# Kernel tuning notes

Measured on AMD Instinct MI355X. Metric: run time of the kernel, lower is better.

Reference implementation:

```python
import jax, jax.numpy as jnp
import numpy as np

B, D = 4, 4            # batch, days
N = 5000               # node_number
V = 256                # congestion_space_dimension
F = 64                 # in_channels
C = 32                 # out_channels per head
H = 4                  # heads
E = 80000              # edges per graph (before self loops)
NEG_SLOPE = 0.2        # PyG GATConv default negative_slope


def setup_inputs() -> dict:
    key = jax.random.key(0)
    ks = jax.random.split(key, 7)
    x = jax.random.randint(ks[0], (B, D, N), 0, V)
    adjacency = jax.random.randint(ks[1], (2, E), 0, N)
    emb = jax.random.normal(ks[2], (V, F), dtype=jnp.float32)
    W = jax.random.normal(ks[3], (F, H * C), dtype=jnp.float32) * 0.1
    att_src = jax.random.normal(ks[4], (H, C), dtype=jnp.float32) * 0.1
    att_dst = jax.random.normal(ks[5], (H, C), dtype=jnp.float32) * 0.1
    bias = jnp.zeros((H * C,), dtype=jnp.float32)
    return {"x": x, "adjacency": adjacency, "emb": emb, "W": W,
            "att_src": att_src, "att_dst": att_dst, "bias": bias}


def reference(x, adjacency, emb, W, att_src, att_dst, bias):
    G = B * D
    feats = emb[x].reshape(G, N, F)                       # [G,N,F] embedding lookup
    # PyG GATConv adds self loops by default
    loops = jnp.arange(N)
    src = jnp.concatenate([adjacency[0], loops])          # [Et]
    dst = jnp.concatenate([adjacency[1], loops])          # [Et]
    xw = jnp.einsum('gnf,fk->gnk', feats, W).reshape(G, N, H, C)
    a_s = jnp.einsum('gnhc,hc->gnh', xw, att_src)         # [G,N,H]
    a_d = jnp.einsum('gnhc,hc->gnh', xw, att_dst)
    e = jax.nn.leaky_relu(a_s[:, src] + a_d[:, dst], NEG_SLOPE)  # [G,Et,H]
    # per-destination segment softmax (stable)
    seg_max = jax.vmap(lambda v: jax.ops.segment_max(v, dst, num_segments=N))(e)
    alpha = jnp.exp(e - seg_max[:, dst])
    denom = jax.vmap(lambda v: jax.ops.segment_sum(v, dst, num_segments=N))(alpha)
    alpha = alpha / denom[:, dst]                         # [G,Et,H]
    msg = alpha[..., None] * xw[:, src]                   # [G,Et,H,C]
    out = jax.vmap(lambda m: jax.ops.segment_sum(m, dst, num_segments=N))(msg)
    out = out.reshape(G, N, H * C) + bias                 # concat heads + bias
    return out.reshape(B, D, N * H * C)
```

## Files before the change

kernel.cpp:

```cpp
#include <hip/hip_runtime.h>
#include <math.h>

#define NN 5000
#define GG 16
#define VV 256
#define FF 64
#define HH 4
#define CC 32
#define HC 128
#define EE 80000
#define NEG 0.2f
#define WPB 4
#define SLOT 48
#define SPAD 50
#define CAP 96
#define NTASK (GG * NN / 4)

__global__ void k_tables(const float* __restrict__ emb, const float* __restrict__ W,
                         const float* __restrict__ att_src, const float* __restrict__ att_dst,
                         float* __restrict__ T, float* __restrict__ as_t, float* __restrict__ ad_t,
                         int* __restrict__ cursor, int* __restrict__ csr) {
  if (blockIdx.x >= VV) {
    int n = (blockIdx.x - VV) * 128 + threadIdx.x;
    if (n < NN) {
      cursor[n] = 1;
      csr[n * CAP] = n;
    }
    return;
  }
  __shared__ float se[FF];
  __shared__ float sT[HC];
  const int v = blockIdx.x;
  const int k = threadIdx.x;
  if (k < FF) se[k] = emb[v * FF + k];
  __syncthreads();
  float acc = 0.f;
#pragma unroll
  for (int f = 0; f < FF; ++f) acc += se[f] * W[f * HC + k];
  T[v * HC + k] = acc;
  sT[k] = acc;
  __syncthreads();
  if (k < 2 * HH) {
    const int h = k >> 1;
    const float* att = (k & 1) ? att_dst : att_src;
    float s = 0.f;
#pragma unroll
    for (int c = 0; c < CC; ++c) s += sT[h * CC + c] * att[h * CC + c];
    if (k & 1) ad_t[v * HH + h] = s;
    else       as_t[v * HH + h] = s;
  }
}

#define NSCAT ((EE + 255) / 256)
__global__ void k_scatter_p(const int* __restrict__ src, const int* __restrict__ dst,
                            int* __restrict__ cursor, int* __restrict__ csr,
                            const float* __restrict__ as_t, const float* __restrict__ ad_t,
                            float* __restrict__ P) {
  if (blockIdx.x < NSCAT) {
    int e = blockIdx.x * 256 + threadIdx.x;
    if (e < EE) {
      int d = dst[e];
      int pos = atomicAdd(&cursor[d], 1);
      if (pos < CAP) csr[d * CAP + pos] = src[e];
    }
    return;
  }
  const int d = blockIdx.x - NSCAT;
  const int v = threadIdx.x;
  const float4 a = ((const float4*)as_t)[v];
  const float4 b = ((const float4*)ad_t)[d];
  float e0 = a.x + b.x; e0 = e0 > 0.f ? e0 : NEG * e0;
  float e1 = a.y + b.y; e1 = e1 > 0.f ? e1 : NEG * e1;
  float e2 = a.z + b.z; e2 = e2 > 0.f ? e2 : NEG * e2;
  float e3 = a.w + b.w; e3 = e3 > 0.f ? e3 : NEG * e3;
  float4 p;
  p.x = __expf(e0); p.y = __expf(e1); p.z = __expf(e2); p.w = __expf(e3);
  ((float4*)P)[d * VV + v] = p;
}

__global__ __launch_bounds__(256)
void k_gat(const int* __restrict__ x, const int* __restrict__ cursor,
           const int* __restrict__ csr, const float* __restrict__ T,
           const float* __restrict__ P, const float* __restrict__ bias,
           float* __restrict__ out) {
  __shared__ float4 s_p4[WPB][4][SPAD];
  __shared__ int    s_ofs[WPB][4][SPAD];

  const int tid  = threadIdx.x;
  const int wave = tid >> 6;
  const int lane = tid & 63;
  const int sub  = lane >> 4;
  const int sl   = lane & 15;
  const int head = sl >> 2;

  const int w    = blockIdx.x * WPB + wave;
  const int inst = w * 4 + sub;
  const int g    = inst / NN;
  const int n    = inst - g * NN;

  const int base = n * CAP;
  const int deg  = min(cursor[n], CAP);
  const int xd   = x[inst];
  const float4* __restrict__ Pd = ((const float4*)P) + xd * VV;
  const int* __restrict__ xg = x + g * NN;

  const int my_ch = sl * 8;
  const float4 b0 = ((const float4*)bias)[sl * 2];
  const float4 b1 = ((const float4*)bias)[sl * 2 + 1];

  float4 dsum = make_float4(0.f, 0.f, 0.f, 0.f);
  float4 a0 = make_float4(0.f, 0.f, 0.f, 0.f);
  float4 a1 = make_float4(0.f, 0.f, 0.f, 0.f);

  for (int c0 = 0; c0 < deg; c0 += SLOT) {
    const int len = min(SLOT, deg - c0);
    for (int r = sl; r < len; r += 16) {
      const int srcn = csr[base + c0 + r];
      const int xv   = xg[srcn];
      const float4 p4 = Pd[xv];
      dsum.x += p4.x; dsum.y += p4.y; dsum.z += p4.z; dsum.w += p4.w;
      s_p4[wave][sub][r]  = p4;
      s_ofs[wave][sub][r] = xv << 7;
    }
    __threadfence_block();
#pragma unroll 2
    for (int j = 0; j < len; ++j) {
      const int   ofs = s_ofs[wave][sub][j];
      const float p   = ((const float*)&s_p4[wave][sub][j])[head];
      const float4 t0 = *(const float4*)&T[ofs + my_ch];
      const float4 t1 = *(const float4*)&T[ofs + my_ch + 4];
      a0.x += p * t0.x; a0.y += p * t0.y; a0.z += p * t0.z; a0.w += p * t0.w;
      a1.x += p * t1.x; a1.y += p * t1.y; a1.z += p * t1.z; a1.w += p * t1.w;
    }
    __threadfence_block();
  }

#pragma unroll
  for (int d = 1; d < 16; d <<= 1) {
    dsum.x += __shfl_xor(dsum.x, d);
    dsum.y += __shfl_xor(dsum.y, d);
    dsum.z += __shfl_xor(dsum.z, d);
    dsum.w += __shfl_xor(dsum.w, d);
  }
  const float den = (head == 0) ? dsum.x : (head == 1) ? dsum.y
                   : (head == 2) ? dsum.z : dsum.w;
  const float r = 1.f / den;

  float4 o0, o1;
  o0.x = a0.x * r + b0.x; o0.y = a0.y * r + b0.y;
  o0.z = a0.z * r + b0.z; o0.w = a0.w * r + b0.w;
  o1.x = a1.x * r + b1.x; o1.y = a1.y * r + b1.y;
  o1.z = a1.z * r + b1.z; o1.w = a1.w * r + b1.w;
  float* op = out + (size_t)inst * HC + my_ch;
  *(float4*)op = o0;
  *(float4*)(op + 4) = o1;
}

extern "C" void kernel_launch(void* const* d_in, const int* in_sizes, int n_in,
                              void* d_out, int out_size, void* d_ws, size_t ws_size,
                              hipStream_t stream) {
  const int*   x       = (const int*)d_in[0];
  const int*   adj     = (const int*)d_in[1];
  const float* emb     = (const float*)d_in[2];
  const float* W       = (const float*)d_in[3];
  const float* att_src = (const float*)d_in[4];
  const float* att_dst = (const float*)d_in[5];
  const float* bias    = (const float*)d_in[6];
  float*       out     = (float*)d_out;

  const int* adj_src = adj;
  const int* adj_dst = adj + EE;

  char* wp = (char*)d_ws;
  float* T    = (float*)wp; wp += (size_t)VV * HC * 4;
  float* as_t = (float*)wp; wp += (size_t)VV * HH * 4;
  float* ad_t = (float*)wp; wp += (size_t)VV * HH * 4;
  int* cursor = (int*)wp;   wp += (size_t)NN * 4;
  int* csr    = (int*)wp;   wp += (size_t)NN * CAP * 4;
  float* P    = (float*)wp; wp += (size_t)VV * VV * HH * 4;

  const int initblk = (NN + 127) / 128;
  k_tables<<<VV + initblk, 128, 0, stream>>>(emb, W, att_src, att_dst,
                                             T, as_t, ad_t, cursor, csr);
  k_scatter_p<<<NSCAT + VV, 256, 0, stream>>>(adj_src, adj_dst, cursor, csr,
                                              as_t, ad_t, P);
  k_gat<<<NTASK / WPB, 256, 0, stream>>>(x, cursor, csr, T, P, bias, out);
}
```

Measured before the change: 125.0 us.

## Stage half of projected table in LDS with persistent grid split by head pairs

The aggregation kernel now runs as a persistent grid of 512 blocks of 1024 threads. Each block loads one half of the 256x128 projected embedding table (two heads, 64 KB) into shared memory and loops over node tasks with a grid stride. Each lane accumulates 4 channels read from LDS instead of 8 channels gathered from global memory. The aim is to turn random global/L2 gathers of T into LDS reads, at the cost of twice the CSR and P gather work (each half-block redoes the weight loads), a 64 KB+ LDS footprint that limits occupancy, and an upfront table copy per block.

```diff
diff --git a/kernel.cpp b/kernel.cpp
--- a/kernel.cpp
+++ b/kernel.cpp
@@ -10,11 +10,13 @@
 #define HC 128
 #define EE 80000
 #define NEG 0.2f
-#define WPB 4
 #define SLOT 48
 #define SPAD 50
 #define CAP 96
 #define NTASK (GG * NN / 4)
+#define TW 16
+#define GRIDB 512
+#define TSTRIDE ((GRIDB / 2) * TW)
 
 __global__ void k_tables(const float* __restrict__ emb, const float* __restrict__ W,
                          const float* __restrict__ att_src, const float* __restrict__ att_dst,
@@ -78,82 +80,87 @@
   ((float4*)P)[d * VV + v] = p;
 }
 
-__global__ __launch_bounds__(256)
+__global__ __launch_bounds__(1024)
 void k_gat(const int* __restrict__ x, const int* __restrict__ cursor,
            const int* __restrict__ csr, const float* __restrict__ T,
            const float* __restrict__ P, const float* __restrict__ bias,
            float* __restrict__ out) {
-  __shared__ float4 s_p4[WPB][4][SPAD];
-  __shared__ int    s_ofs[WPB][4][SPAD];
+  __shared__ float  sT[VV * 64];
+  __shared__ float4 s_p4[TW][4][SPAD];
+  __shared__ int    s_ofs[TW][4][SPAD];
 
-  const int tid  = threadIdx.x;
+  const int tid = threadIdx.x;
+  const int hf  = blockIdx.x & 1;
+
+  {
+    const float4* __restrict__ Tg4 = (const float4*)T;
+    float4* sT4 = (float4*)sT;
+    for (int i = tid; i < VV * 16; i += 1024) {
+      const int v = i >> 4, c4 = i & 15;
+      sT4[i] = Tg4[v * 32 + hf * 16 + c4];
+    }
+  }
+  __syncthreads();
+
   const int wave = tid >> 6;
   const int lane = tid & 63;
   const int sub  = lane >> 4;
   const int sl   = lane & 15;
-  const int head = sl >> 2;
+  const int head = hf * 2 + (sl >> 3);
 
-  const int w    = blockIdx.x * WPB + wave;
-  const int inst = w * 4 + sub;
-  const int g    = inst / NN;
-  const int n    = inst - g * NN;
+  const float4 b0 = ((const float4*)bias)[hf * 16 + sl];
 
-  const int base = n * CAP;
-  const int deg  = min(cursor[n], CAP);
-  const int xd   = x[inst];
-  const float4* __restrict__ Pd = ((const float4*)P) + xd * VV;
-  const int* __restrict__ xg = x + g * NN;
+  for (int t = (blockIdx.x >> 1) * TW + wave; t < NTASK; t += TSTRIDE) {
+    const int inst = t * 4 + sub;
+    const int g    = inst / NN;
+    const int n    = inst - g * NN;
 
-  const int my_ch = sl * 8;
-  const float4 b0 = ((const float4*)bias)[sl * 2];
-  const float4 b1 = ((const float4*)bias)[sl * 2 + 1];
+    const int base = n * CAP;
+    const int deg  = min(cursor[n], CAP);
+    const int xd   = x[inst];
+    const float4* __restrict__ Pd = ((const float4*)P) + xd * VV;
+    const int* __restrict__ xg = x + g * NN;
 
-  float4 dsum = make_float4(0.f, 0.f, 0.f, 0.f);
-  float4 a0 = make_float4(0.f, 0.f, 0.f, 0.f);
-  float4 a1 = make_float4(0.f, 0.f, 0.f, 0.f);
+    float4 dsum = make_float4(0.f, 0.f, 0.f, 0.f);
+    float4 a0 = make_float4(0.f, 0.f, 0.f, 0.f);
 
-  for (int c0 = 0; c0 < deg; c0 += SLOT) {
-    const int len = min(SLOT, deg - c0);
-    for (int r = sl; r < len; r += 16) {
-      const int srcn = csr[base + c0 + r];
-      const int xv   = xg[srcn];
-      const float4 p4 = Pd[xv];
-      dsum.x += p4.x; dsum.y += p4.y; dsum.z += p4.z; dsum.w += p4.w;
-      s_p4[wave][sub][r]  = p4;
-      s_ofs[wave][sub][r] = xv << 7;
+    for (int c0 = 0; c0 < deg; c0 += SLOT) {
+      const int len = min(SLOT, deg - c0);
+      for (int r = sl; r < len; r += 16) {
+        const int srcn = csr[base + c0 + r];
+        const int xv   = xg[srcn];
+        const float4 p4 = Pd[xv];
+        dsum.x += p4.x; dsum.y += p4.y; dsum.z += p4.z; dsum.w += p4.w;
+        s_p4[wave][sub][r]  = p4;
+        s_ofs[wave][sub][r] = xv << 6;
+      }
+      __threadfence_block();
+#pragma unroll 4
+      for (int j = 0; j < len; ++j) {
+        const int   ofs = s_ofs[wave][sub][j];
+        const float p   = ((const float*)&s_p4[wave][sub][j])[head];
+        const float4 t0 = *(const float4*)&sT[ofs + sl * 4];
+        a0.x += p * t0.x; a0.y += p * t0.y; a0.z += p * t0.z; a0.w += p * t0.w;
+      }
+      __threadfence_block();
     }
-    __threadfence_block();
-#pragma unroll 2
-    for (int j = 0; j < len; ++j) {
-      const int   ofs = s_ofs[wave][sub][j];
-      const float p   = ((const float*)&s_p4[wave][sub][j])[head];
-      const float4 t0 = *(const float4*)&T[ofs + my_ch];
-      const float4 t1 = *(const float4*)&T[ofs + my_ch + 4];
-      a0.x += p * t0.x; a0.y += p * t0.y; a0.z += p * t0.z; a0.w += p * t0.w;
-      a1.x += p * t1.x; a1.y += p * t1.y; a1.z += p * t1.z; a1.w += p * t1.w;
-    }
-    __threadfence_block();
-  }
 
 #pragma unroll
-  for (int d = 1; d < 16; d <<= 1) {
-    dsum.x += __shfl_xor(dsum.x, d);
-    dsum.y += __shfl_xor(dsum.y, d);
-    dsum.z += __shfl_xor(dsum.z, d);
-    dsum.w += __shfl_xor(dsum.w, d);
+    for (int d = 1; d < 16; d <<= 1) {
+      dsum.x += __shfl_xor(dsum.x, d);
+      dsum.y += __shfl_xor(dsum.y, d);
+      dsum.z += __shfl_xor(dsum.z, d);
+      dsum.w += __shfl_xor(dsum.w, d);
+    }
+    const float den = hf ? ((sl & 8) ? dsum.w : dsum.z)
+                         : ((sl & 8) ? dsum.y : dsum.x);
+    const float r = 1.f / den;
+
+    float4 o;
+    o.x = a0.x * r + b0.x; o.y = a0.y * r + b0.y;
+    o.z = a0.z * r + b0.z; o.w = a0.w * r + b0.w;
+    *(float4*)&out[(size_t)inst * HC + hf * 64 + sl * 4] = o;
   }
-  const float den = (head == 0) ? dsum.x : (head == 1) ? dsum.y
-                   : (head == 2) ? dsum.z : dsum.w;
-  const float r = 1.f / den;
-
-  float4 o0, o1;
-  o0.x = a0.x * r + b0.x; o0.y = a0.y * r + b0.y;
-  o0.z = a0.z * r + b0.z; o0.w = a0.w * r + b0.w;
-  o1.x = a1.x * r + b1.x; o1.y = a1.y * r + b1.y;
-  o1.z = a1.z * r + b1.z; o1.w = a1.w * r + b1.w;
-  float* op = out + (size_t)inst * HC + my_ch;
-  *(float4*)op = o0;
-  *(float4*)(op + 4) = o1;
 }
 
 extern "C" void kernel_launch(void* const* d_in, const int* in_sizes, int n_in,
@@ -184,5 +191,5 @@
                                              T, as_t, ad_t, cursor, csr);
   k_scatter_p<<<NSCAT + VV, 256, 0, stream>>>(adj_src, adj_dst, cursor, csr,
                                               as_t, ad_t, P);
-  k_gat<<<NTASK / WPB, 256, 0, stream>>>(x, cursor, csr, T, P, bias, out);
+  k_gat<<<GRIDB, 1024, 0, stream>>>(x, cursor, csr, T, P, bias, out);
 }
```

New measurement: 150.9 us. +20.7%, slower.

## Store T table in fp16 and remap GAT work to node-major half-wave tasks

Applied to the files above, without the earlier changes.

The projected embedding table T is now stored as fp16, halving its footprint and gather bandwidth. The GAT kernel is restructured so each wave serves one node across two graphs, 32 lanes per graph with 4 channels per lane. Every lane now loads the CSR index, the source token and the P value directly, replacing the shared-memory staging and shuffle reduction of the denominator. Because all 8 waves that share a node read the same CSR row, that row should stay in cache. The cost is fp16 rounding error in the output and redundant per-lane index and P loads.

```diff
diff --git a/kernel.cpp b/kernel.cpp
--- a/kernel.cpp
+++ b/kernel.cpp
@@ -1,4 +1,5 @@
 #include <hip/hip_runtime.h>
+#include <hip/hip_fp16.h>
 #include <math.h>
 
 #define NN 5000
@@ -10,15 +11,12 @@
 #define HC 128
 #define EE 80000
 #define NEG 0.2f
-#define WPB 4
-#define SLOT 48
-#define SPAD 50
 #define CAP 96
-#define NTASK (GG * NN / 4)
 
 __global__ void k_tables(const float* __restrict__ emb, const float* __restrict__ W,
                          const float* __restrict__ att_src, const float* __restrict__ att_dst,
-                         float* __restrict__ T, float* __restrict__ as_t, float* __restrict__ ad_t,
+                         __half* __restrict__ T16, float* __restrict__ as_t,
+                         float* __restrict__ ad_t,
                          int* __restrict__ cursor, int* __restrict__ csr) {
   if (blockIdx.x >= VV) {
     int n = (blockIdx.x - VV) * 128 + threadIdx.x;
@@ -37,7 +35,7 @@
   float acc = 0.f;
 #pragma unroll
   for (int f = 0; f < FF; ++f) acc += se[f] * W[f * HC + k];
-  T[v * HC + k] = acc;
+  T16[v * HC + k] = __float2half(acc);
   sT[k] = acc;
   __syncthreads();
   if (k < 2 * HH) {
@@ -80,80 +78,49 @@
 
 __global__ __launch_bounds__(256)
 void k_gat(const int* __restrict__ x, const int* __restrict__ cursor,
-           const int* __restrict__ csr, const float* __restrict__ T,
+           const int* __restrict__ csr, const __half* __restrict__ T16,
            const float* __restrict__ P, const float* __restrict__ bias,
            float* __restrict__ out) {
-  __shared__ float4 s_p4[WPB][4][SPAD];
-  __shared__ int    s_ofs[WPB][4][SPAD];
-
   const int tid  = threadIdx.x;
   const int wave = tid >> 6;
   const int lane = tid & 63;
-  const int sub  = lane >> 4;
-  const int sl   = lane & 15;
-  const int head = sl >> 2;
-
-  const int w    = blockIdx.x * WPB + wave;
-  const int inst = w * 4 + sub;
-  const int g    = inst / NN;
-  const int n    = inst - g * NN;
+  const int t    = blockIdx.x * 4 + wave;
+  const int n    = t >> 3;
+  const int gp   = t & 7;
+  const int g    = gp * 2 + (lane >> 5);
+  const int cl   = lane & 31;
+  const int c4   = cl * 4;
+  const int head = cl >> 3;
 
   const int base = n * CAP;
   const int deg  = min(cursor[n], CAP);
-  const int xd   = x[inst];
-  const float4* __restrict__ Pd = ((const float4*)P) + xd * VV;
   const int* __restrict__ xg = x + g * NN;
+  const int xd   = xg[n];
+  const float* __restrict__ Pg = P + ((size_t)xd << 10) + head;
 
-  const int my_ch = sl * 8;
-  const float4 b0 = ((const float4*)bias)[sl * 2];
-  const float4 b1 = ((const float4*)bias)[sl * 2 + 1];
+  float4 acc = make_float4(0.f, 0.f, 0.f, 0.f);
+  float dsum = 0.f;
 
-  float4 dsum = make_float4(0.f, 0.f, 0.f, 0.f);
-  float4 a0 = make_float4(0.f, 0.f, 0.f, 0.f);
-  float4 a1 = make_float4(0.f, 0.f, 0.f, 0.f);
-
-  for (int c0 = 0; c0 < deg; c0 += SLOT) {
-    const int len = min(SLOT, deg - c0);
-    for (int r = sl; r < len; r += 16) {
-      const int srcn = csr[base + c0 + r];
-      const int xv   = xg[srcn];
-      const float4 p4 = Pd[xv];
-      dsum.x += p4.x; dsum.y += p4.y; dsum.z += p4.z; dsum.w += p4.w;
-      s_p4[wave][sub][r]  = p4;
-      s_ofs[wave][sub][r] = xv << 7;
-    }
-    __threadfence_block();
 #pragma unroll 2
-    for (int j = 0; j < len; ++j) {
-      const int   ofs = s_ofs[wave][sub][j];
-      const float p   = ((const float*)&s_p4[wave][sub][j])[head];
-      const float4 t0 = *(const float4*)&T[ofs + my_ch];
-      const float4 t1 = *(const float4*)&T[ofs + my_ch + 4];
-      a0.x += p * t0.x; a0.y += p * t0.y; a0.z += p * t0.z; a0.w += p * t0.w;
-      a1.x += p * t1.x; a1.y += p * t1.y; a1.z += p * t1.z; a1.w += p * t1.w;
-    }
-    __threadfence_block();
+  for (int j = 0; j < deg; ++j) {
+    const int srcn = csr[base + j];
+    const int xv   = xg[srcn];
+    const float p  = Pg[(size_t)xv << 2];
+    union { uint2 u; __half2 h2[2]; } tt;
+    tt.u = *(const uint2*)&T16[((size_t)xv << 7) + c4];
+    const float2 lo = __half22float2(tt.h2[0]);
+    const float2 hi = __half22float2(tt.h2[1]);
+    acc.x += p * lo.x; acc.y += p * lo.y;
+    acc.z += p * hi.x; acc.w += p * hi.y;
+    dsum += p;
   }
 
-#pragma unroll
-  for (int d = 1; d < 16; d <<= 1) {
-    dsum.x += __shfl_xor(dsum.x, d);
-    dsum.y += __shfl_xor(dsum.y, d);
-    dsum.z += __shfl_xor(dsum.z, d);
-    dsum.w += __shfl_xor(dsum.w, d);
-  }
-  const float den = (head == 0) ? dsum.x : (head == 1) ? dsum.y
-                   : (head == 2) ? dsum.z : dsum.w;
-  const float r = 1.f / den;
-
-  float4 o0, o1;
-  o0.x = a0.x * r + b0.x; o0.y = a0.y * r + b0.y;
-  o0.z = a0.z * r + b0.z; o0.w = a0.w * r + b0.w;
-  o1.x = a1.x * r + b1.x; o1.y = a1.y * r + b1.y;
-  o1.z = a1.z * r + b1.z; o1.w = a1.w * r + b1.w;
-  float* op = out + (size_t)inst * HC + my_ch;
-  *(float4*)op = o0;
-  *(float4*)(op + 4) = o1;
+  const float r = 1.f / dsum;
+  const float4 b4 = ((const float4*)bias)[cl];
+  float4 o;
+  o.x = acc.x * r + b4.x; o.y = acc.y * r + b4.y;
+  o.z = acc.z * r + b4.z; o.w = acc.w * r + b4.w;
+  *(float4*)&out[((size_t)(g * NN + n)) * HC + c4] = o;
 }
 
 extern "C" void kernel_launch(void* const* d_in, const int* in_sizes, int n_in,
@@ -172,17 +139,17 @@
   const int* adj_dst = adj + EE;
 
   char* wp = (char*)d_ws;
-  float* T    = (float*)wp; wp += (size_t)VV * HC * 4;
-  float* as_t = (float*)wp; wp += (size_t)VV * HH * 4;
-  float* ad_t = (float*)wp; wp += (size_t)VV * HH * 4;
-  int* cursor = (int*)wp;   wp += (size_t)NN * 4;
-  int* csr    = (int*)wp;   wp += (size_t)NN * CAP * 4;
-  float* P    = (float*)wp; wp += (size_t)VV * VV * HH * 4;
+  __half* T16 = (__half*)wp; wp += (size_t)VV * HC * 2;
+  float* as_t = (float*)wp;  wp += (size_t)VV * HH * 4;
+  float* ad_t = (float*)wp;  wp += (size_t)VV * HH * 4;
+  int* cursor = (int*)wp;    wp += (size_t)NN * 4;
+  int* csr    = (int*)wp;    wp += (size_t)NN * CAP * 4;
+  float* P    = (float*)wp;  wp += (size_t)VV * VV * HH * 4;
 
   const int initblk = (NN + 127) / 128;
   k_tables<<<VV + initblk, 128, 0, stream>>>(emb, W, att_src, att_dst,
-                                             T, as_t, ad_t, cursor, csr);
+                                             T16, as_t, ad_t, cursor, csr);
   k_scatter_p<<<NSCAT + VV, 256, 0, stream>>>(adj_src, adj_dst, cursor, csr,
                                               as_t, ad_t, P);
-  k_gat<<<NTASK / WPB, 256, 0, stream>>>(x, cursor, csr, T, P, bias, out);
+  k_gat<<<NN * 8 / 4, 256, 0, stream>>>(x, cursor, csr, T16, P, bias, out);
 }
```

New measurement: 135.3 us. 8.2% more time.
